# Kernel optimization log

Hardware: AMD Instinct MI355X
Metric: run time of the kernel (lower is better)

## Reference

```python
import jax, jax.numpy as jnp
import numpy as np

B, T, N, DIN, D = 8, 20, 1000, 64, 64


def setup_inputs() -> dict:
    key = jax.random.key(0)
    ks = jax.random.split(key, 10)
    stdv = 1.0 / np.sqrt(DIN + D)  # torch reset_param: uniform(-1/sqrt(in_size), ...)
    def gate_w(k):
        return jax.random.uniform(k, (N, DIN + D, D), jnp.float32, -stdv, stdv)
    x = jax.random.normal(ks[0], (B, T, N, DIN), jnp.float32)
    # xavier_normal_ for time_att.W [N, T, D]: fan_in=T*D, fan_out=N*D
    xav_std = np.sqrt(2.0 / (T * D + N * D)).astype(np.float32)
    Wt = jax.random.normal(ks[5], (N, T, D), jnp.float32) * xav_std
    return {
        "x": x,
        "Wi": gate_w(ks[1]), "bi": jnp.zeros((N, D), jnp.float32),
        "Wo": gate_w(ks[2]), "bo": jnp.zeros((N, D), jnp.float32),
        "Wf": gate_w(ks[3]), "bf": jnp.zeros((N, D), jnp.float32),
        "Wc": gate_w(ks[4]), "bc": jnp.zeros((N, D), jnp.float32),
        "Wt": Wt,
    }


def _lstm_att(x, Wi, bi, Wo, bo, Wf, bf, Wc, bc, Wt):
    b, t, n, din = x.shape
    d = Wi.shape[-1]

    def gate(xh, W, bias):
        # per-stock matmul: [b,n,din+d] x [n,din+d,d] -> [b,n,d]
        return jnp.einsum('bni,nio->bno', xh, W) + bias

    def step(carry, xt):
        h, c = carry  # [b,n,d]
        xh = jnp.concatenate([xt, h], axis=-1)
        it = jax.nn.sigmoid(gate(xh, Wi, bi))
        ot = jax.nn.sigmoid(gate(xh, Wo, bo))
        ft = jax.nn.sigmoid(gate(xh, Wf, bf))
        ch = jnp.tanh(gate(xh, Wc, bc))
        c2 = ft * c + it * ch
        h2 = ot * jnp.tanh(c2)
        return (h2, c2), h2

    h0 = jnp.zeros((b, n, d), x.dtype)
    c0 = jnp.zeros((b, n, d), x.dtype)
    xt_seq = jnp.swapaxes(x, 0, 1)  # [t,b,n,din]
    _, hs = jax.lax.scan(step, (h0, c0), xt_seq)
    h = jnp.swapaxes(hs, 0, 1)  # [b,t,n,d] (torch.stack dim=-3)

    # time attention
    h_bntd = jnp.swapaxes(h, 1, 2)  # [b,n,t,d]
    scores = jnp.sum(h_bntd * Wt, axis=-1)  # [b,n,t]
    att = jax.nn.softmax(scores, axis=-1)
    out = jnp.einsum('bnt,bntd->bnd', att, h_bntd)  # matmul([b,n,1,t],[b,n,t,d]).squeeze()
    return out  # [b,n,d]


def reference(x, Wi, bi, Wo, bo, Wf, bf, Wc, bc, Wt):
    return _lstm_att(x, Wi, bi, Wo, bo, Wf, bf, Wc, bc, Wt)
```

## Files before the change

### kernel.cpp

```cpp
#include <hip/hip_runtime.h>

#define TT 20
#define NSTK 1000
#define THREADS 256

typedef float f32x4 __attribute__((ext_vector_type(4)));
typedef _Float16 f16x8 __attribute__((ext_vector_type(8)));
typedef _Float16 f16x2 __attribute__((ext_vector_type(2)));

__device__ __forceinline__ float rcp_f(float x) { return __builtin_amdgcn_rcpf(x); }
__device__ __forceinline__ float sigmoid_f(float x) { return rcp_f(1.0f + __expf(-x)); }
__device__ __forceinline__ float tanh_f(float x) {
    return 1.0f - 2.0f * rcp_f(__expf(2.0f * x) + 1.0f);
}

#define AIDX(kf, q, row, j) ((((kf) * 4 + (q)) * 16 + (row)) * 8 + (j))

extern "C" __global__ void __launch_bounds__(THREADS, 4)
lstm_att_f16(const float* __restrict__ x,
             const float* __restrict__ Wi, const float* __restrict__ bi,
             const float* __restrict__ Wo, const float* __restrict__ bo,
             const float* __restrict__ Wf, const float* __restrict__ bf_,
             const float* __restrict__ Wc, const float* __restrict__ bc,
             const float* __restrict__ Wt,
             float* __restrict__ out)
{
    __shared__ __align__(16) _Float16 afrag[2][2048];
    __shared__ __align__(16) _Float16 hhist[TT * 8 * 64];

    const int n    = blockIdx.x;
    const int tid  = threadIdx.x;
    const int lane = tid & 63;
    const int w    = tid >> 6;
    const int q    = lane >> 4;
    const int r16  = lane & 15;
    const int dcol = w * 16 + r16;
    const bool hi  = lane >= 32;
    const int rowbase = ((lane & 31) >> 4) * 4 + (hi ? 2 : 0);

    f16x8 bw[4][4];
    {
        const float* Wg[4] = {Wi, Wo, Wf, Wc};
        #pragma unroll
        for (int g = 0; g < 4; ++g) {
            const float* base = Wg[g] + (size_t)n * 8192 + dcol;
            #pragma unroll
            for (int kf = 0; kf < 4; ++kf)
                #pragma unroll
                for (int j = 0; j < 8; ++j)
                    bw[g][kf][j] = (_Float16)base[(kf * 32 + q * 8 + j) * 64];
        }
    }
    float biasv[4];
    biasv[0] = bi[n * 64 + dcol];
    biasv[1] = bo[n * 64 + dcol];
    biasv[2] = bf_[n * 64 + dcol];
    biasv[3] = bc[n * 64 + dcol];

    const int sb = tid >> 5, dx = (tid & 31) * 2;
    const int sbase = AIDX(dx >> 5, (dx & 31) >> 3, sb, dx & 7);
    const float* xptr = x + ((size_t)sb * TT * NSTK + (size_t)n) * 64 + dx;

    {
        const float2 x0 = *(const float2*)xptr;
        *(f16x2*)(&afrag[0][sbase]) = (f16x2){(_Float16)x0.x, (_Float16)x0.y};
        #pragma unroll
        for (int u = 0; u < 4; ++u)
            afrag[0][1024 + tid + u * THREADS] = (_Float16)0.0f;
    }
    float2 xreg = *(const float2*)(xptr + (size_t)NSTK * 64);

    float cst0 = 0.f, cst1 = 0.f;

    __syncthreads();

    const int kfh = 2 + (dcol >> 5), kkh = dcol & 31;
    const int hb0 = AIDX(kfh, kkh >> 3, rowbase, kkh & 7);

    for (int t = 0; t < TT; ++t) {
        const int cur = t & 1, nxt = cur ^ 1;

        f16x8 af[4];
        #pragma unroll
        for (int kf = 0; kf < 4; ++kf)
            af[kf] = *(const f16x8*)(&afrag[cur][AIDX(kf, q, r16, 0)]);

        if (t + 1 < TT)
            *(f16x2*)(&afrag[nxt][sbase]) = (f16x2){(_Float16)xreg.x, (_Float16)xreg.y};
        {
            const int tn = (t + 2 < TT) ? t + 2 : TT - 1;
            xreg = *(const float2*)(xptr + (size_t)tn * NSTK * 64);
        }

        f32x4 acc[4];
        #pragma unroll
        for (int g = 0; g < 4; ++g)
            acc[g] = (f32x4){biasv[g], biasv[g], biasv[g], biasv[g]};
        #pragma unroll
        for (int kf = 0; kf < 4; ++kf) {
            #pragma unroll
            for (int g = 0; g < 4; ++g)
                acc[g] = __builtin_amdgcn_mfma_f32_16x16x32_f16(af[kf], bw[g][kf], acc[g], 0, 0, 0);
        }

        float p0[4], p1[4];
        #pragma unroll
        for (int g = 0; g < 4; ++g) {
            const float t2 = __shfl_xor(acc[g][2], 32, 64);
            const float t3 = __shfl_xor(acc[g][3], 32, 64);
            p0[g] = hi ? t2 : acc[g][0];
            p1[g] = hi ? t3 : acc[g][1];
        }

        const float ig0 = sigmoid_f(p0[0]), og0 = sigmoid_f(p0[1]);
        const float fg0 = sigmoid_f(p0[2]), cg0 = tanh_f(p0[3]);
        const float ig1 = sigmoid_f(p1[0]), og1 = sigmoid_f(p1[1]);
        const float fg1 = sigmoid_f(p1[2]), cg1 = tanh_f(p1[3]);
        cst0 = fmaf(fg0, cst0, ig0 * cg0);
        cst1 = fmaf(fg1, cst1, ig1 * cg1);
        const float h0 = og0 * tanh_f(cst0);
        const float h1 = og1 * tanh_f(cst1);

        afrag[nxt][hb0]     = (_Float16)h0;
        afrag[nxt][hb0 + 8] = (_Float16)h1;
        hhist[(t * 8 + rowbase) * 64 + dcol]     = (_Float16)h0;
        hhist[(t * 8 + rowbase + 1) * 64 + dcol] = (_Float16)h1;

        __syncthreads();
    }

    const float* wtg = Wt + (size_t)n * (TT * 64);
    #pragma unroll
    for (int bb = 0; bb < 2; ++bb) {
        const int b = 2 * w + bb;
        float s[TT];
        #pragma unroll
        for (int t = 0; t < TT; ++t)
            s[t] = (float)hhist[(t * 8 + b) * 64 + lane] * wtg[t * 64 + lane];
        #pragma unroll
        for (int t = 0; t < TT; ++t) {
            #pragma unroll
            for (int mk = 32; mk >= 1; mk >>= 1)
                s[t] += __shfl_xor(s[t], mk, 64);
        }
        float m = s[0];
        #pragma unroll
        for (int t = 1; t < TT; ++t) m = fmaxf(m, s[t]);
        float se = 0.f;
        #pragma unroll
        for (int t = 0; t < TT; ++t) { s[t] = __expf(s[t] - m); se += s[t]; }
        const float rs = rcp_f(se);
        float o = 0.f;
        #pragma unroll
        for (int t = 0; t < TT; ++t)
            o = fmaf(s[t], (float)hhist[(t * 8 + b) * 64 + lane], o);
        out[((size_t)b * NSTK + n) * 64 + lane] = o * rs;
    }
}

extern "C" void kernel_launch(void* const* d_in, const int* in_sizes, int n_in,
                              void* d_out, int out_size, void* d_ws, size_t ws_size,
                              hipStream_t stream) {
    const float* x  = (const float*)d_in[0];
    const float* Wi = (const float*)d_in[1];
    const float* bi = (const float*)d_in[2];
    const float* Wo = (const float*)d_in[3];
    const float* bo = (const float*)d_in[4];
    const float* Wf = (const float*)d_in[5];
    const float* bf = (const float*)d_in[6];
    const float* Wc = (const float*)d_in[7];
    const float* bc = (const float*)d_in[8];
    const float* Wt = (const float*)d_in[9];
    float* out = (float*)d_out;

    lstm_att_f16<<<NSTK, THREADS, 0, stream>>>(
        x, Wi, bi, Wo, bo, Wf, bf, Wc, bc, Wt, out);
}
```

Before: 56.91 us.

## Preload full x sequence into LDS and fold exp2 scaling into weights

```diff
diff --git a/kernel.cpp b/kernel.cpp
--- a/kernel.cpp
+++ b/kernel.cpp
@@ -3,30 +3,30 @@
 #define TT 20
 #define NSTK 1000
 #define THREADS 256
+#define XP 72
+
+#define SC_SIG  1.44269504089f
+#define SC_TANH 2.88539008178f
 
 typedef float f32x4 __attribute__((ext_vector_type(4)));
 typedef _Float16 f16x8 __attribute__((ext_vector_type(8)));
 typedef _Float16 f16x2 __attribute__((ext_vector_type(2)));
 
 __device__ __forceinline__ float rcp_f(float x) { return __builtin_amdgcn_rcpf(x); }
-__device__ __forceinline__ float sigmoid_f(float x) { return rcp_f(1.0f + __expf(-x)); }
-__device__ __forceinline__ float tanh_f(float x) {
-    return 1.0f - 2.0f * rcp_f(__expf(2.0f * x) + 1.0f);
-}
+__device__ __forceinline__ float exp2_f(float x) { return __builtin_amdgcn_exp2f(x); }
 
-#define AIDX(kf, q, row, j) ((((kf) * 4 + (q)) * 16 + (row)) * 8 + (j))
 
-extern "C" __global__ void __launch_bounds__(THREADS, 4)
-lstm_att_f16(const float* __restrict__ x,
-             const float* __restrict__ Wi, const float* __restrict__ bi,
-             const float* __restrict__ Wo, const float* __restrict__ bo,
-             const float* __restrict__ Wf, const float* __restrict__ bf_,
-             const float* __restrict__ Wc, const float* __restrict__ bc,
-             const float* __restrict__ Wt,
-             float* __restrict__ out)
+extern "C" __global__ void __launch_bounds__(THREADS, 3)
+lstm_att_lean(const float* __restrict__ x,
+              const float* __restrict__ Wi, const float* __restrict__ bi,
+              const float* __restrict__ Wo, const float* __restrict__ bo,
+              const float* __restrict__ Wf, const float* __restrict__ bf_,
+              const float* __restrict__ Wc, const float* __restrict__ bc,
+              const float* __restrict__ Wt,
+              float* __restrict__ out)
 {
-    __shared__ __align__(16) _Float16 afrag[2][2048];
-    __shared__ __align__(16) _Float16 hhist[TT * 8 * 64];
+    __shared__ __align__(16) _Float16 xs[TT][8][XP];
+    __shared__ __align__(16) _Float16 hh[TT + 1][8][XP];
 
     const int n    = blockIdx.x;
     const int tid  = threadIdx.x;
@@ -34,63 +34,55 @@
     const int w    = tid >> 6;
     const int q    = lane >> 4;
     const int r16  = lane & 15;
+    const int brow = r16 & 7;
     const int dcol = w * 16 + r16;
     const bool hi  = lane >= 32;
     const int rowbase = ((lane & 31) >> 4) * 4 + (hi ? 2 : 0);
 
+    const int xrow = tid >> 5;
+    const int xd   = (tid & 31) * 2;
+    float2 xr[TT];
+    #pragma unroll
+    for (int u = 0; u < TT; ++u) {
+        const int r = u * 8 + xrow;
+        xr[u] = *(const float2*)(x + ((size_t)r * NSTK + n) * 64 + xd);
+    }
+
     f16x8 bw[4][4];
+    float biasv[4];
     {
         const float* Wg[4] = {Wi, Wo, Wf, Wc};
+        const float* Bg[4] = {bi, bo, bf_, bc};
         #pragma unroll
         for (int g = 0; g < 4; ++g) {
+            const float sc = (g == 3) ? SC_TANH : SC_SIG;
             const float* base = Wg[g] + (size_t)n * 8192 + dcol;
             #pragma unroll
             for (int kf = 0; kf < 4; ++kf)
                 #pragma unroll
                 for (int j = 0; j < 8; ++j)
-                    bw[g][kf][j] = (_Float16)base[(kf * 32 + q * 8 + j) * 64];
+                    bw[g][kf][j] = (_Float16)(base[(kf * 32 + q * 8 + j) * 64] * sc);
+            biasv[g] = Bg[g][n * 64 + dcol] * sc;
         }
     }
-    float biasv[4];
-    biasv[0] = bi[n * 64 + dcol];
-    biasv[1] = bo[n * 64 + dcol];
-    biasv[2] = bf_[n * 64 + dcol];
-    biasv[3] = bc[n * 64 + dcol];
 
-    const int sb = tid >> 5, dx = (tid & 31) * 2;
-    const int sbase = AIDX(dx >> 5, (dx & 31) >> 3, sb, dx & 7);
-    const float* xptr = x + ((size_t)sb * TT * NSTK + (size_t)n) * 64 + dx;
-
-    {
-        const float2 x0 = *(const float2*)xptr;
-        *(f16x2*)(&afrag[0][sbase]) = (f16x2){(_Float16)x0.x, (_Float16)x0.y};
-        #pragma unroll
-        for (int u = 0; u < 4; ++u)
-            afrag[0][1024 + tid + u * THREADS] = (_Float16)0.0f;
+    #pragma unroll
+    for (int u = 0; u < TT; ++u) {
+        const int r = u * 8 + xrow;
+        const int b = r / TT, t = r % TT;
+        *(f16x2*)(&xs[t][b][xd]) = (f16x2){(_Float16)xr[u].x, (_Float16)xr[u].y};
     }
-    float2 xreg = *(const float2*)(xptr + (size_t)NSTK * 64);
+    for (int i = tid; i < 8 * XP / 2; i += THREADS) ((unsigned*)hh)[i] = 0u;
 
     float cst0 = 0.f, cst1 = 0.f;
-
     __syncthreads();
 
-    const int kfh = 2 + (dcol >> 5), kkh = dcol & 31;
-    const int hb0 = AIDX(kfh, kkh >> 3, rowbase, kkh & 7);
-
     for (int t = 0; t < TT; ++t) {
-        const int cur = t & 1, nxt = cur ^ 1;
-
         f16x8 af[4];
-        #pragma unroll
-        for (int kf = 0; kf < 4; ++kf)
-            af[kf] = *(const f16x8*)(&afrag[cur][AIDX(kf, q, r16, 0)]);
-
-        if (t + 1 < TT)
-            *(f16x2*)(&afrag[nxt][sbase]) = (f16x2){(_Float16)xreg.x, (_Float16)xreg.y};
-        {
-            const int tn = (t + 2 < TT) ? t + 2 : TT - 1;
-            xreg = *(const float2*)(xptr + (size_t)tn * NSTK * 64);
-        }
+        af[0] = *(const f16x8*)(&xs[t][brow][q * 8]);
+        af[1] = *(const f16x8*)(&xs[t][brow][32 + q * 8]);
+        af[2] = *(const f16x8*)(&hh[t][brow][q * 8]);
+        af[3] = *(const f16x8*)(&hh[t][brow][32 + q * 8]);
 
         f32x4 acc[4];
         #pragma unroll
@@ -112,19 +104,21 @@
             p1[g] = hi ? t3 : acc[g][1];
         }
 
-        const float ig0 = sigmoid_f(p0[0]), og0 = sigmoid_f(p0[1]);
-        const float fg0 = sigmoid_f(p0[2]), cg0 = tanh_f(p0[3]);
-        const float ig1 = sigmoid_f(p1[0]), og1 = sigmoid_f(p1[1]);
-        const float fg1 = sigmoid_f(p1[2]), cg1 = tanh_f(p1[3]);
+        const float ig0 = rcp_f(1.0f + exp2_f(-p0[0]));
+        const float og0 = rcp_f(1.0f + exp2_f(-p0[1]));
+        const float fg0 = rcp_f(1.0f + exp2_f(-p0[2]));
+        const float cg0 = 1.0f - 2.0f * rcp_f(exp2_f(p0[3]) + 1.0f);
+        const float ig1 = rcp_f(1.0f + exp2_f(-p1[0]));
+        const float og1 = rcp_f(1.0f + exp2_f(-p1[1]));
+        const float fg1 = rcp_f(1.0f + exp2_f(-p1[2]));
+        const float cg1 = 1.0f - 2.0f * rcp_f(exp2_f(p1[3]) + 1.0f);
         cst0 = fmaf(fg0, cst0, ig0 * cg0);
         cst1 = fmaf(fg1, cst1, ig1 * cg1);
-        const float h0 = og0 * tanh_f(cst0);
-        const float h1 = og1 * tanh_f(cst1);
+        const float h0 = og0 * (1.0f - 2.0f * rcp_f(exp2_f(cst0 * SC_TANH) + 1.0f));
+        const float h1 = og1 * (1.0f - 2.0f * rcp_f(exp2_f(cst1 * SC_TANH) + 1.0f));
 
-        afrag[nxt][hb0]     = (_Float16)h0;
-        afrag[nxt][hb0 + 8] = (_Float16)h1;
-        hhist[(t * 8 + rowbase) * 64 + dcol]     = (_Float16)h0;
-        hhist[(t * 8 + rowbase + 1) * 64 + dcol] = (_Float16)h1;
+        hh[t + 1][rowbase][dcol]     = (_Float16)h0;
+        hh[t + 1][rowbase + 1][dcol] = (_Float16)h1;
 
         __syncthreads();
     }
@@ -136,7 +130,7 @@
         float s[TT];
         #pragma unroll
         for (int t = 0; t < TT; ++t)
-            s[t] = (float)hhist[(t * 8 + b) * 64 + lane] * wtg[t * 64 + lane];
+            s[t] = (float)hh[t + 1][b][lane] * wtg[t * 64 + lane];
         #pragma unroll
         for (int t = 0; t < TT; ++t) {
             #pragma unroll
@@ -148,12 +142,12 @@
         for (int t = 1; t < TT; ++t) m = fmaxf(m, s[t]);
         float se = 0.f;
         #pragma unroll
-        for (int t = 0; t < TT; ++t) { s[t] = __expf(s[t] - m); se += s[t]; }
+        for (int t = 0; t < TT; ++t) { s[t] = exp2_f((s[t] - m) * SC_SIG); se += s[t]; }
         const float rs = rcp_f(se);
         float o = 0.f;
         #pragma unroll
         for (int t = 0; t < TT; ++t)
-            o = fmaf(s[t], (float)hhist[(t * 8 + b) * 64 + lane], o);
+            o = fmaf(s[t], (float)hh[t + 1][b][lane], o);
         out[((size_t)b * NSTK + n) * 64 + lane] = o * rs;
     }
 }
@@ -173,6 +167,6 @@
     const float* Wt = (const float*)d_in[9];
     float* out = (float*)d_out;
 
-    lstm_att_f16<<<NSTK, THREADS, 0, stream>>>(
+    lstm_att_lean<<<NSTK, THREADS, 0, stream>>>(
         x, Wi, bi, Wo, bo, Wf, bf, Wc, bc, Wt, out);
 }
```

Result: slower. 68.81 us (+20.9%).
